# Performance work log

Hardware: AMD Instinct MI355X
Metric: run time of the kernel (lower is better)

The kernel has to match this reference:

```python
import jax, jax.numpy as jnp
import numpy as np

N = 50000      # num nodes
E = 800000     # num edges
IN = 512       # in_feats (= num_hidden)
H = 8          # num_heads
D = 64         # out_feats per head (H*D = 512)
NEG_SLOPE = 0.2


def setup_inputs() -> dict:
    key = jax.random.key(0)
    ks = jax.random.split(key, 7)
    feat = jax.random.normal(ks[0], (N, IN), jnp.float32)
    src = jax.random.randint(ks[1], (E,), 0, N)
    dst = jax.random.randint(ks[2], (E,), 0, N)
    W_fc = jax.random.normal(ks[3], (IN, H * D), jnp.float32) * (1.0 / np.sqrt(IN))
    W_res = jax.random.normal(ks[4], (IN, H * D), jnp.float32) * (1.0 / np.sqrt(IN))
    attn_l = jax.random.normal(ks[5], (1, H, D), jnp.float32) * 0.1
    attn_r = jax.random.normal(ks[6], (1, H, D), jnp.float32) * 0.1
    return {"feat": feat, "src": src, "dst": dst, "W_fc": W_fc,
            "W_res": W_res, "attn_l": attn_l, "attn_r": attn_r}


def reference(feat, src, dst, W_fc, W_res, attn_l, attn_r):
    # fc: [N, IN] @ [IN, H*D] -> [N, H, D]
    ft = (feat @ W_fc).reshape(N, H, D)
    # attention logits per node: el = sum(ft * attn_l, -1), er likewise -> [N, H]
    el = jnp.sum(ft * attn_l, axis=-1)
    er = jnp.sum(ft * attn_r, axis=-1)
    # u_add_v on edges, then LeakyReLU -> [E, H]
    e = jax.nn.leaky_relu(el[src] + er[dst], negative_slope=NEG_SLOPE)
    # edge_softmax: normalize over incoming edges of each dst node
    m = jax.ops.segment_max(e, dst, num_segments=N)            # [N, H]
    m = jnp.where(jnp.isfinite(m), m, jnp.zeros_like(m))       # guard zero-in-degree
    ex = jnp.exp(e - m[dst])                                   # [E, H]
    s = jax.ops.segment_sum(ex, dst, num_segments=N)           # [N, H]
    a = ex / jnp.maximum(s[dst], 1e-9)                         # [E, H]
    # u_mul_e + sum aggregation: gather src features, weight, scatter-add to dst
    msg = ft[src] * a[:, :, None]                              # [E, H, D]
    rst = jax.ops.segment_sum(msg, dst, num_segments=N)        # [N, H, D]
    # residual: res_fc Linear since in_dst_feats != out_feats
    rst = rst + (feat @ W_res).reshape(N, H, D)
    return rst
```

## Files before the change

kernel.cpp:

```cpp
#include <hip/hip_runtime.h>
#include <hip/hip_bf16.h>

#define NN 50000
#define EE 800000
#define INF 512
#define HH 8
#define DD 64
#define HD 512
#define NTOT 1024

typedef unsigned short u16;
typedef u16 u16x8 __attribute__((ext_vector_type(8)));
typedef __bf16 bf16x8 __attribute__((ext_vector_type(8)));
typedef float f32x4 __attribute__((ext_vector_type(4)));

__device__ __forceinline__ float bf2f(u16 u) {
    return __uint_as_float(((unsigned)u) << 16);
}
__device__ __forceinline__ u16 f2bf(float f) {
    __hip_bfloat16 h = __float2bfloat16(f);
    return *reinterpret_cast<u16*>(&h);
}

__device__ __forceinline__ void gload_lds16(const void* g, void* l) {
    __builtin_amdgcn_global_load_lds(
        (const __attribute__((address_space(1))) void*)g,
        (__attribute__((address_space(3))) void*)l, 16, 0, 0);
}

__global__ __launch_bounds__(256) void sniff5_kernel(const u16* __restrict__ p0,
                                                     const u16* __restrict__ p1,
                                                     const u16* __restrict__ p2,
                                                     const u16* __restrict__ p3,
                                                     const u16* __restrict__ p4,
                                                     int* __restrict__ flags) {
    const u16* ps[5] = {p0, p1, p2, p3, p4};
    const u16* p = ps[blockIdx.x];
    __shared__ int bad;
    if (threadIdx.x == 0) bad = 0;
    __syncthreads();
    float v = fabsf(bf2f(p[2 * threadIdx.x]));
    if (!(v < 1e4f)) atomicAdd(&bad, 1);
    __syncthreads();
    if (threadIdx.x == 0) flags[blockIdx.x] = (bad >= 8) ? 1 : 0;
}

__global__ __launch_bounds__(256) void transpose_kernel(const void* __restrict__ in,
                                                        u16* __restrict__ out,
                                                        const int* __restrict__ flag) {
    __shared__ u16 tile[64][65];
    const int isf32 = *flag;
    int tr = (blockIdx.x & 7) * 64;
    int tc = (blockIdx.x >> 3) * 64;
    for (int idx = threadIdx.x; idx < 64 * 64; idx += 256) {
        int r = idx >> 6, c = idx & 63;
        int g = (tr + r) * 512 + tc + c;
        tile[r][c] = isf32 ? f2bf(((const float*)in)[g]) : ((const u16*)in)[g];
    }
    __syncthreads();
    for (int idx = threadIdx.x; idx < 64 * 64; idx += 256) {
        int r = idx >> 6, c = idx & 63;
        out[(tc + r) * 512 + tr + c] = tile[c][r];
    }
}

__global__ void zero_deg_kernel(int* __restrict__ deg) {
    int t = blockIdx.x * 256 + threadIdx.x;
    if (t < NN) deg[t] = 0;
}

__global__ void count_kernel(const int* __restrict__ dst, int* __restrict__ deg) {
    int e = blockIdx.x * 256 + threadIdx.x;
    if (e < EE) atomicAdd(&deg[dst[e]], 1);
}

#define SCAN_CH 49
__global__ __launch_bounds__(1024) void scan_kernel(const int* __restrict__ deg,
                                                    int* __restrict__ rowptr,
                                                    int* __restrict__ cursor) {
    __shared__ int sums[1024];
    int t = threadIdx.x;
    int base = t * SCAN_CH;
    int s = 0;
    for (int k = 0; k < SCAN_CH; ++k) {
        int i = base + k;
        if (i < NN) s += deg[i];
    }
    sums[t] = s;
    __syncthreads();
    for (int off = 1; off < 1024; off <<= 1) {
        int v = (t >= off) ? sums[t - off] : 0;
        __syncthreads();
        sums[t] += v;
        __syncthreads();
    }
    int run = (t == 0) ? 0 : sums[t - 1];
    for (int k = 0; k < SCAN_CH; ++k) {
        int i = base + k;
        if (i < NN) {
            rowptr[i] = run;
            cursor[i] = run;
            run += deg[i];
        }
    }
    if (t == 0) rowptr[NN] = EE;
}

__global__ void scatter_kernel(const int* __restrict__ src, const int* __restrict__ dst,
                               int* __restrict__ cursor, int* __restrict__ csr_src) {
    int e = blockIdx.x * 256 + threadIdx.x;
    if (e < EE) {
        int p = atomicAdd(&cursor[dst[e]], 1);
        csr_src[p] = src[e];
    }
}

#define TM 128
#define TN 128
#define BK 64
#define NMBLK 392

__global__ __launch_bounds__(256) void gemm_kernel(const void* __restrict__ A,
                                                   const u16* __restrict__ Wt,
                                                   u16* __restrict__ ft,
                                                   float* __restrict__ outf,
                                                   const int* __restrict__ flag) {
    __shared__ char smem[TM * BK * 4 + TN * BK * 2];
    float* Asf = (float*)smem;
    u16*   As16 = (u16*)smem;
    u16*   Bs = (u16*)(smem + TM * BK * 4);

    const int isf32 = *flag;
    const int bid = blockIdx.x;
    const int r8 = bid & 7;
    const int q = bid >> 3;
    const int m0 = (((q >> 3) << 3) | r8) * TM;
    const int n0 = (q & 7) * TN;
    const int tid = threadIdx.x;
    const int lane = tid & 63;
    const int wave = tid >> 6;
    const int wr = (wave >> 1) * 64;
    const int wc = (wave & 1) * 64;
    const int lrow = lane & 15;
    const int quad = lane >> 4;

    f32x4 acc[4][4] = {};

    for (int k0 = 0; k0 < INF; k0 += BK) {
        __syncthreads();
        if (isf32) {
            const float* Af = (const float*)A;
            int rg = lane >> 4;
            int ch = (lane & 15) >> 1;
            int hf = lane & 1;
#pragma unroll
            for (int g = 0; g < 8; ++g) {
                int G = wave * 8 + g;
                int r = G * 4 + rg;
                int cs = ch ^ (r & 7);
                int gr = m0 + r; gr = gr < NN ? gr : NN - 1;
                gload_lds16(Af + (size_t)gr * INF + k0 + cs * 8 + hf * 4,
                            Asf + G * 256);
            }
        } else {
            const u16* Ab = (const u16*)A;
            int rg = lane >> 3;
            int ch = lane & 7;
#pragma unroll
            for (int g = 0; g < 4; ++g) {
                int G = wave * 4 + g;
                int r = G * 8 + rg;
                int cs = ch ^ (r & 7);
                int gr = m0 + r; gr = gr < NN ? gr : NN - 1;
                gload_lds16(Ab + (size_t)gr * INF + k0 + cs * 8,
                            As16 + G * 512);
            }
        }
        {
            int rg = lane >> 3;
            int ch = lane & 7;
#pragma unroll
            for (int g = 0; g < 4; ++g) {
                int G = wave * 4 + g;
                int r = G * 8 + rg;
                int cs = ch ^ (r & 7);
                gload_lds16(Wt + (size_t)(n0 + r) * INF + k0 + cs * 8,
                            Bs + G * 512);
            }
        }
        __syncthreads();

#pragma unroll
        for (int ks = 0; ks < 2; ++ks) {
            bf16x8 af[4], bfr[4];
            if (isf32) {
#pragma unroll
                for (int mi = 0; mi < 4; ++mi) {
                    int ar = wr + mi * 16 + lrow;
                    int sc = (ks * 4 + quad) ^ (ar & 7);
                    const f32x4* p = (const f32x4*)(Asf + ar * 64 + sc * 8);
                    f32x4 lo = p[0], hi = p[1];
                    u16x8 t;
#pragma unroll
                    for (int j = 0; j < 4; ++j) { t[j] = f2bf(lo[j]); t[4 + j] = f2bf(hi[j]); }
                    af[mi] = *(bf16x8*)&t;
                }
            } else {
#pragma unroll
                for (int mi = 0; mi < 4; ++mi) {
                    int ar = wr + mi * 16 + lrow;
                    int sc = (ks * 4 + quad) ^ (ar & 7);
                    u16x8 t = *(const u16x8*)(As16 + ar * 64 + sc * 8);
                    af[mi] = *(bf16x8*)&t;
                }
            }
#pragma unroll
            for (int ni = 0; ni < 4; ++ni) {
                int br = wc + ni * 16 + lrow;
                int sc = (ks * 4 + quad) ^ (br & 7);
                u16x8 t = *(const u16x8*)(Bs + br * 64 + sc * 8);
                bfr[ni] = *(bf16x8*)&t;
            }
#pragma unroll
            for (int mi = 0; mi < 4; ++mi)
#pragma unroll
                for (int ni = 0; ni < 4; ++ni)
                    acc[mi][ni] = __builtin_amdgcn_mfma_f32_16x16x32_bf16(af[mi], bfr[ni],
                                                                          acc[mi][ni], 0, 0, 0);
        }
    }

#pragma unroll
    for (int mi = 0; mi < 4; ++mi) {
        int rb = m0 + wr + mi * 16 + quad * 4;
#pragma unroll
        for (int ni = 0; ni < 4; ++ni) {
            int col = n0 + wc + ni * 16 + lrow;
#pragma unroll
            for (int r = 0; r < 4; ++r) {
                int row = rb + r;
                if (row < NN) {
                    float v = acc[mi][ni][r];
                    if (col < HD) ft[row * HD + col] = f2bf(v);
                    else outf[row * HD + (col - HD)] = v;
                }
            }
        }
    }
}

__global__ __launch_bounds__(256) void attn_dot_kernel(const u16* __restrict__ ft,
                                                       const void* __restrict__ al,
                                                       const void* __restrict__ ar,
                                                       float* __restrict__ el,
                                                       float* __restrict__ er,
                                                       const int* __restrict__ flags) {
    int node = blockIdx.x * 4 + (threadIdx.x >> 6);
    if (node >= NN) return;
    int lane = threadIdx.x & 63;
    int off = lane * 8;

    float wl[8], wr_[8];
    if (flags[3]) {
        f32x4 a0 = *(const f32x4*)((const float*)al + off);
        f32x4 a1 = *(const f32x4*)((const float*)al + off + 4);
#pragma unroll
        for (int j = 0; j < 4; ++j) { wl[j] = a0[j]; wl[4 + j] = a1[j]; }
    } else {
        u16x8 a = *(const u16x8*)((const u16*)al + off);
#pragma unroll
        for (int j = 0; j < 8; ++j) wl[j] = bf2f(a[j]);
    }
    if (flags[4]) {
        f32x4 a0 = *(const f32x4*)((const float*)ar + off);
        f32x4 a1 = *(const f32x4*)((const float*)ar + off + 4);
#pragma unroll
        for (int j = 0; j < 4; ++j) { wr_[j] = a0[j]; wr_[4 + j] = a1[j]; }
    } else {
        u16x8 a = *(const u16x8*)((const u16*)ar + off);
#pragma unroll
        for (int j = 0; j < 8; ++j) wr_[j] = bf2f(a[j]);
    }

    u16x8 f = *(const u16x8*)(ft + node * HD + off);
    float vl = 0.0f, vr = 0.0f;
#pragma unroll
    for (int j = 0; j < 8; ++j) {
        float x = bf2f(f[j]);
        vl += x * wl[j];
        vr += x * wr_[j];
    }
#pragma unroll
    for (int msk = 1; msk < 8; msk <<= 1) {
        vl += __shfl_xor(vl, msk);
        vr += __shfl_xor(vr, msk);
    }
    if ((lane & 7) == 0) {
        el[node * HH + (lane >> 3)] = vl;
        er[node * HH + (lane >> 3)] = vr;
    }
}

__global__ __launch_bounds__(256) void aggregate_kernel(const int* __restrict__ rowptr,
                                                        const int* __restrict__ csr_src,
                                                        const u16* __restrict__ ft,
                                                        const float* __restrict__ el,
                                                        const float* __restrict__ er,
                                                        float* __restrict__ outf) {
    int node = blockIdx.x * 4 + (threadIdx.x >> 6);
    if (node >= NN) return;
    int lane = threadIdx.x & 63;
    int head = lane >> 3;
    int beg = rowptr[node], end = rowptr[node + 1];
    float erd = er[node * HH + head];

    float m = -INFINITY;
    float sden = 0.0f;
    float acc[8] = {};

    float el_n = 0.0f;
    u16x8 f_n = {};
    if (beg < end) {
        int s0 = csr_src[beg];
        el_n = el[s0 * HH + head];
        f_n = *(const u16x8*)(ft + s0 * HD + lane * 8);
    }
    for (int i = beg; i < end; ++i) {
        float elv = el_n;
        u16x8 f = f_n;
        if (i + 1 < end) {
            int s2 = csr_src[i + 1];
            el_n = el[s2 * HH + head];
            f_n = *(const u16x8*)(ft + s2 * HD + lane * 8);
        }
        float v = elv + erd;
        v = v > 0.0f ? v : 0.2f * v;
        float nm = fmaxf(m, v);
        float scale = __expf(m - nm);
        float ex = __expf(v - nm);
        m = nm;
        sden = sden * scale + ex;
#pragma unroll
        for (int j = 0; j < 8; ++j) acc[j] = acc[j] * scale + bf2f(f[j]) * ex;
    }

    float inv = 1.0f / fmaxf(sden, 1e-9f);
    float* op = outf + node * HD + lane * 8;
    f32x4 r0 = *(const f32x4*)op;
    f32x4 r1 = *(const f32x4*)(op + 4);
    f32x4 o0, o1;
#pragma unroll
    for (int j = 0; j < 4; ++j) {
        o0[j] = acc[j] * inv + r0[j];
        o1[j] = acc[4 + j] * inv + r1[j];
    }
    *(f32x4*)op = o0;
    *(f32x4*)(op + 4) = o1;
}

extern "C" void kernel_launch(void* const* d_in, const int* in_sizes, int n_in,
                              void* d_out, int out_size, void* d_ws, size_t ws_size,
                              hipStream_t stream) {
    const void* feat   = d_in[0];
    const int*  src    = (const int*)d_in[1];
    const int*  dst    = (const int*)d_in[2];
    const void* W_fc   = d_in[3];
    const void* W_res  = d_in[4];
    const void* attn_l = d_in[5];
    const void* attn_r = d_in[6];
    float* outf = (float*)d_out;

    char* ws = (char*)d_ws;
    int*   flags   = (int*)(ws);
    u16*   Wt      = (u16*)(ws + 256);
    u16*   ft      = (u16*)(ws + 1048832);
    float* el      = (float*)(ws + 52248832);
    float* er      = (float*)(ws + 53848832);
    int*   deg     = (int*)(ws + 55448832);
    int*   rowptr  = (int*)(ws + 55648832);
    int*   cursor  = (int*)(ws + 55848896);
    int*   csr_src = (int*)(ws + 56048896);

    sniff5_kernel<<<5, 256, 0, stream>>>((const u16*)feat, (const u16*)W_fc,
                                         (const u16*)W_res, (const u16*)attn_l,
                                         (const u16*)attn_r, flags);
    transpose_kernel<<<64, 256, 0, stream>>>(W_fc, Wt, flags + 1);
    transpose_kernel<<<64, 256, 0, stream>>>(W_res, Wt + 512 * 512, flags + 2);

    zero_deg_kernel<<<(NN + 255) / 256, 256, 0, stream>>>(deg);
    count_kernel<<<(EE + 255) / 256, 256, 0, stream>>>(dst, deg);
    scan_kernel<<<1, 1024, 0, stream>>>(deg, rowptr, cursor);
    scatter_kernel<<<(EE + 255) / 256, 256, 0, stream>>>(src, dst, cursor, csr_src);

    gemm_kernel<<<NMBLK * 8, 256, 0, stream>>>(feat, Wt, ft, outf, flags + 0);

    attn_dot_kernel<<<(NN + 3) / 4, 256, 0, stream>>>(ft, attn_l, attn_r, el, er, flags);
    aggregate_kernel<<<(NN + 3) / 4, 256, 0, stream>>>(rowptr, csr_src, ft, el, er, outf);
}
```

Baseline: 672.9 us.

## Double-buffer GEMM tiles and convert A to bf16 before LDS staging

Restructures the fused fc/residual GEMM into a two-stage software pipeline: the next K tile of A is loaded into registers and the next B tile is sent asynchronously into a second LDS buffer while MFMAs run on the current buffer. A is now converted from fp32 to bf16 once, at LDS write time, instead of being converted by every wave at fragment-read time. This also halves LDS usage for A. It aims to hide global-load latency and remove redundant conversion work. The cost is extra register pressure from the staged A values and one barrier per iteration.

New measurement: 700.9 us. +4.2%, slower.

```diff
diff --git a/kernel.cpp b/kernel.cpp
--- a/kernel.cpp
+++ b/kernel.cpp
@@ -118,6 +118,7 @@
 #define TM 128
 #define TN 128
 #define BK 64
+#define NT (INF / BK)
 #define NMBLK 392
 
 __global__ __launch_bounds__(256) void gemm_kernel(const void* __restrict__ A,
@@ -125,10 +126,8 @@
                                                    u16* __restrict__ ft,
                                                    float* __restrict__ outf,
                                                    const int* __restrict__ flag) {
-    __shared__ char smem[TM * BK * 4 + TN * BK * 2];
-    float* Asf = (float*)smem;
-    u16*   As16 = (u16*)smem;
-    u16*   Bs = (u16*)(smem + TM * BK * 4);
+    __shared__ u16 Asm[2][TM * BK];
+    __shared__ u16 Bsm[2][TN * BK];
 
     const int isf32 = *flag;
     const int bid = blockIdx.x;
@@ -144,82 +143,81 @@
     const int lrow = lane & 15;
     const int quad = lane >> 4;
 
+    const int ar_ = tid >> 1;
+    const int ah_ = tid & 1;
+    int gr = m0 + ar_;
+    gr = gr < NN ? gr : NN - 1;
+    const float* Af = (const float*)A + (size_t)gr * INF + ah_ * 32;
+    const u16*   Ab = (const u16*)A + (size_t)gr * INF + ah_ * 32;
+
+    const int rg = lane >> 3;
+    const int ch = lane & 7;
+    const int bcs = ch ^ rg;
+
     f32x4 acc[4][4] = {};
 
-    for (int k0 = 0; k0 < INF; k0 += BK) {
-        __syncthreads();
+    f32x4 a_f[8];
+    u16x8 a_b[4];
+
+    auto issueA = [&](int t) {
+        int k0 = t * BK;
         if (isf32) {
-            const float* Af = (const float*)A;
-            int rg = lane >> 4;
-            int ch = (lane & 15) >> 1;
-            int hf = lane & 1;
-#pragma unroll
-            for (int g = 0; g < 8; ++g) {
-                int G = wave * 8 + g;
-                int r = G * 4 + rg;
-                int cs = ch ^ (r & 7);
-                int gr = m0 + r; gr = gr < NN ? gr : NN - 1;
-                gload_lds16(Af + (size_t)gr * INF + k0 + cs * 8 + hf * 4,
-                            Asf + G * 256);
+#pragma unroll
+            for (int j = 0; j < 8; ++j)
+                a_f[j] = *(const f32x4*)(Af + k0 + j * 4);
+        } else {
+#pragma unroll
+            for (int j = 0; j < 4; ++j)
+                a_b[j] = *(const u16x8*)(Ab + k0 + j * 8);
+        }
+    };
+    auto issueB = [&](int t, int nb) {
+        int k0 = t * BK;
+#pragma unroll
+        for (int g = 0; g < 4; ++g) {
+            int G = wave * 4 + g;
+            int r = G * 8 + rg;
+            gload_lds16(Wt + (size_t)(n0 + r) * INF + k0 + bcs * 8,
+                        &Bsm[nb][G * 512]);
+        }
+    };
+    auto writeA = [&](int nb) {
+        u16x8 w[4];
+        if (isf32) {
+#pragma unroll
+            for (int j = 0; j < 4; ++j) {
+                f32x4 lo = a_f[2 * j], hi = a_f[2 * j + 1];
+#pragma unroll
+                for (int k = 0; k < 4; ++k) { w[j][k] = f2bf(lo[k]); w[j][4 + k] = f2bf(hi[k]); }
             }
         } else {
-            const u16* Ab = (const u16*)A;
-            int rg = lane >> 3;
-            int ch = lane & 7;
-#pragma unroll
-            for (int g = 0; g < 4; ++g) {
-                int G = wave * 4 + g;
-                int r = G * 8 + rg;
-                int cs = ch ^ (r & 7);
-                int gr = m0 + r; gr = gr < NN ? gr : NN - 1;
-                gload_lds16(Ab + (size_t)gr * INF + k0 + cs * 8,
-                            As16 + G * 512);
-            }
-        }
-        {
-            int rg = lane >> 3;
-            int ch = lane & 7;
-#pragma unroll
-            for (int g = 0; g < 4; ++g) {
-                int G = wave * 4 + g;
-                int r = G * 8 + rg;
-                int cs = ch ^ (r & 7);
-                gload_lds16(Wt + (size_t)(n0 + r) * INF + k0 + cs * 8,
-                            Bs + G * 512);
-            }
-        }
-        __syncthreads();
-
+#pragma unroll
+            for (int j = 0; j < 4; ++j) w[j] = a_b[j];
+        }
+#pragma unroll
+        for (int j = 0; j < 4; ++j) {
+            int c = ah_ * 4 + j;
+            int sc = c ^ (ar_ & 7);
+            *(u16x8*)&Asm[nb][ar_ * 64 + sc * 8] = w[j];
+        }
+    };
+    auto compute = [&](int nb) {
 #pragma unroll
         for (int ks = 0; ks < 2; ++ks) {
             bf16x8 af[4], bfr[4];
-            if (isf32) {
-#pragma unroll
-                for (int mi = 0; mi < 4; ++mi) {
-                    int ar = wr + mi * 16 + lrow;
-                    int sc = (ks * 4 + quad) ^ (ar & 7);
-                    const f32x4* p = (const f32x4*)(Asf + ar * 64 + sc * 8);
-                    f32x4 lo = p[0], hi = p[1];
-                    u16x8 t;
-#pragma unroll
-                    for (int j = 0; j < 4; ++j) { t[j] = f2bf(lo[j]); t[4 + j] = f2bf(hi[j]); }
-                    af[mi] = *(bf16x8*)&t;
-                }
-            } else {
-#pragma unroll
-                for (int mi = 0; mi < 4; ++mi) {
-                    int ar = wr + mi * 16 + lrow;
-                    int sc = (ks * 4 + quad) ^ (ar & 7);
-                    u16x8 t = *(const u16x8*)(As16 + ar * 64 + sc * 8);
-                    af[mi] = *(bf16x8*)&t;
-                }
+#pragma unroll
+            for (int mi = 0; mi < 4; ++mi) {
+                int ar = wr + mi * 16 + lrow;
+                int sc = (ks * 4 + quad) ^ (ar & 7);
+                u16x8 tv = *(const u16x8*)&Asm[nb][ar * 64 + sc * 8];
+                af[mi] = *(bf16x8*)&tv;
             }
 #pragma unroll
             for (int ni = 0; ni < 4; ++ni) {
                 int br = wc + ni * 16 + lrow;
                 int sc = (ks * 4 + quad) ^ (br & 7);
-                u16x8 t = *(const u16x8*)(Bs + br * 64 + sc * 8);
-                bfr[ni] = *(bf16x8*)&t;
+                u16x8 tv = *(const u16x8*)&Bsm[nb][br * 64 + sc * 8];
+                bfr[ni] = *(bf16x8*)&tv;
             }
 #pragma unroll
             for (int mi = 0; mi < 4; ++mi)
@@ -228,6 +226,22 @@
                     acc[mi][ni] = __builtin_amdgcn_mfma_f32_16x16x32_bf16(af[mi], bfr[ni],
                                                                           acc[mi][ni], 0, 0, 0);
         }
+    };
+
+    issueA(0);
+    issueB(0, 0);
+    writeA(0);
+    __syncthreads();
+
+    for (int t = 0; t < NT; ++t) {
+        int cur = t & 1;
+        if (t + 1 < NT) {
+            issueA(t + 1);
+            issueB(t + 1, cur ^ 1);
+        }
+        compute(cur);
+        if (t + 1 < NT) writeA(cur ^ 1);
+        __syncthreads();
     }
 
 #pragma unroll
```
